# Kernel optimization log

Hardware: AMD Instinct MI355X
Metric: run time of the kernel (lower is better)

The kernel has to match this reference:

```python
import jax, jax.numpy as jnp
import numpy as np

B = 8192      # n_trials
N = 4096      # network size
N_IN = 3      # input channels (1 osc + 2 stim)
TAU = 0.1
DT = 0.0005


def setup_inputs() -> dict:
    key = jax.random.key(0)
    ks = jax.random.split(key, 8)
    k_t = jax.random.normal(ks[0], (B, 2), dtype=jnp.float32)
    phase = jax.random.uniform(ks[1], (B,), dtype=jnp.float32) * 2.0 * np.pi
    monodromy = jnp.tile(jnp.eye(2, dtype=jnp.float32)[None], (B, 1, 1))
    dK_norms = jnp.zeros((B,), dtype=jnp.float32)
    amp = jnp.float32(1.5)
    w = jnp.float32(2.0 * np.pi * 4.0)  # reference oscillation frequency
    stim = jax.random.normal(ks[2], (N_IN - 1,), dtype=jnp.float32)
    alpha = jax.random.normal(ks[3], (2, N_IN), dtype=jnp.float32)
    I = jax.random.normal(ks[4], (N_IN, N), dtype=jnp.float32)
    m = jax.random.normal(ks[5], (2, N), dtype=jnp.float32)
    n = jax.random.normal(ks[6], (2, N), dtype=jnp.float32)
    return {"k_t": k_t, "phase": phase, "monodromy": monodromy,
            "dK_norms": dK_norms, "amp": amp, "w": w, "stim": stim,
            "alpha": alpha, "I": I, "m": m, "n": n}


def reference(k_t, phase, monodromy, dK_norms, amp, w, stim, alpha, I, m, n):
    # calc_x_u
    tau_sw = w * TAU
    v_osc = amp / jnp.sqrt(1.0 + tau_sw ** 2) * jnp.sin(phase - jnp.arctan2(tau_sw, 1.0))  # [B]
    u_osc = amp * jnp.sin(phase)                                                           # [B]
    u_stim = jnp.broadcast_to(stim[None, :], (phase.shape[0], stim.shape[0]))              # [B, n_in-1]
    u = jnp.concatenate([u_osc[:, None], u_stim], axis=-1)                                  # [B, n_in]
    v = jnp.concatenate([v_osc[:, None], u_stim], axis=-1)                                  # [B, n_in]
    x = k_t @ m + v @ I                                                                     # [B, N]
    tx = jnp.tanh(x)
    # dKdt
    dK = (1.0 / TAU) * (-k_t + tx @ n.T / N + u @ alpha.T)                                  # [B, 2]
    # Jacobian: (1/tau) * (-I2 + (1/N) * einsum over neurons)
    dphi = 1.0 - tx ** 2                                                                    # [B, N]
    Jac = (1.0 / TAU) * (-jnp.eye(2, dtype=x.dtype)[None]
                         + jnp.einsum('bn,kn,dn->bkd', dphi, m, n) / N)                     # [B, 2, 2]
    # Euler update
    k_out = k_t + DT * dK
    phase_out = phase + DT * w
    mono_out = monodromy + DT * jnp.einsum('bkd,bde->bke', Jac, monodromy)
    dK_norms_out = dK_norms + jnp.linalg.norm(dK, axis=-1)
    return (k_out, phase_out, mono_out, dK_norms_out)
```

## Files before the change

### kernel.cpp

```cpp
#include <hip/hip_runtime.h>
#include <math.h>

#define N_SIZE 4096
#define B_SIZE 8192
#define T 4
#define NHALF 2048

typedef float v2f __attribute__((ext_vector_type(2)));

__device__ __forceinline__ float wave_sum(float v) {
#pragma unroll
    for (int off = 32; off >= 1; off >>= 1)
        v += __shfl_xor(v, off, 64);
    return v;
}

__device__ __forceinline__ v2f tanh2(v2f x) {
    v2f xe = x * 2.885390081777927f;
    v2f ex;
    ex.x = __builtin_amdgcn_exp2f(xe.x);
    ex.y = __builtin_amdgcn_exp2f(xe.y);
    v2f d = ex + 1.0f;
    v2f r;
    r.x = __builtin_amdgcn_rcpf(d.x);
    r.y = __builtin_amdgcn_rcpf(d.y);
    return 1.0f - 2.0f * r;
}

__global__ __launch_bounds__(1024)
void bif_kernel(const float* __restrict__ k_t,
                const float* __restrict__ phase,
                const float* __restrict__ mono,
                const float* __restrict__ dKn,
                const float* __restrict__ amp_p,
                const float* __restrict__ w_p,
                const float* __restrict__ stim,
                const float* __restrict__ alpha,
                const float* __restrict__ Im,
                const float* __restrict__ mm,
                const float* __restrict__ nm,
                float* __restrict__ out) {
    __shared__ float s_m0[N_SIZE], s_m1[N_SIZE], s_n0[N_SIZE], s_n1[N_SIZE];
    __shared__ float s_I0[N_SIZE], s_cv[N_SIZE];
    __shared__ float s_red[8 * 2 * 6 * T];

    const int tid  = threadIdx.x;
    const int lane = tid & 63;
    const int wvi  = tid >> 6;
    const int g    = wvi >> 1;
    const int h    = wvi & 1;
    const int b0   = blockIdx.x * 32 + g * T;

    const float st0 = stim[0];
    const float st1 = stim[1];

    {
        const int t4 = tid * 4;
        *(float4*)&s_m0[t4] = *(const float4*)&mm[t4];
        *(float4*)&s_m1[t4] = *(const float4*)&mm[N_SIZE + t4];
        *(float4*)&s_n0[t4] = *(const float4*)&nm[t4];
        *(float4*)&s_n1[t4] = *(const float4*)&nm[N_SIZE + t4];
        *(float4*)&s_I0[t4] = *(const float4*)&Im[t4];
        float4 i1 = *(const float4*)&Im[N_SIZE + t4];
        float4 i2 = *(const float4*)&Im[2 * N_SIZE + t4];
        float4 cv;
        cv.x = st0 * i1.x + st1 * i2.x;
        cv.y = st0 * i1.y + st1 * i2.y;
        cv.z = st0 * i1.z + st1 * i2.z;
        cv.w = st0 * i1.w + st1 * i2.w;
        *(float4*)&s_cv[t4] = cv;
    }

    const float amp = amp_p[0];
    const float w   = w_p[0];
    const float tau_sw = w * 0.1f;
    const float phi0 = atanf(tau_sw);
    const float vamp = amp / sqrtf(1.0f + tau_sw * tau_sw);

    float k0[T], k1[T], vo[T];
#pragma unroll
    for (int t = 0; t < T; ++t) {
        const int b = b0 + t;
        k0[t] = k_t[2 * b];
        k1[t] = k_t[2 * b + 1];
        vo[t] = vamp * sinf(phase[b] - phi0);
    }

    __syncthreads();

    v2f As0[T] = {}, As1[T] = {};
    v2f A00[T] = {}, A01[T] = {};
    v2f A10[T] = {}, A11[T] = {};

    const int base = h * NHALF;
#pragma unroll 2
    for (int it = 0; it < NHALF / 256; ++it) {
        const int j = base + it * 256 + lane * 4;
        float4 fm0 = *(const float4*)&s_m0[j];
        float4 fm1 = *(const float4*)&s_m1[j];
        float4 fn0 = *(const float4*)&s_n0[j];
        float4 fn1 = *(const float4*)&s_n1[j];
        float4 fi0 = *(const float4*)&s_I0[j];
        float4 fcv = *(const float4*)&s_cv[j];
        v2f Ms0[2] = {{fm0.x, fm0.y}, {fm0.z, fm0.w}};
        v2f Ms1[2] = {{fm1.x, fm1.y}, {fm1.z, fm1.w}};
        v2f Nn0[2] = {{fn0.x, fn0.y}, {fn0.z, fn0.w}};
        v2f Nn1[2] = {{fn1.x, fn1.y}, {fn1.z, fn1.w}};
        v2f Iv[2]  = {{fi0.x, fi0.y}, {fi0.z, fi0.w}};
        v2f Cv[2]  = {{fcv.x, fcv.y}, {fcv.z, fcv.w}};
#pragma unroll
        for (int p = 0; p < 2; ++p) {
#pragma unroll
            for (int t = 0; t < T; ++t) {
                v2f x  = Cv[p] + k0[t] * Ms0[p] + k1[t] * Ms1[p] + vo[t] * Iv[p];
                v2f tx = tanh2(x);
                v2f dphi = 1.0f - tx * tx;
                v2f a0 = dphi * Ms0[p];
                v2f a1 = dphi * Ms1[p];
                As0[t] += tx * Nn0[p];
                As1[t] += tx * Nn1[p];
                A00[t] += a0 * Nn0[p];
                A01[t] += a0 * Nn1[p];
                A10[t] += a1 * Nn0[p];
                A11[t] += a1 * Nn1[p];
            }
        }
    }

#pragma unroll
    for (int t = 0; t < T; ++t) {
        float r0 = wave_sum(As0[t].x + As0[t].y);
        float r1 = wave_sum(As1[t].x + As1[t].y);
        float r2 = wave_sum(A00[t].x + A00[t].y);
        float r3 = wave_sum(A01[t].x + A01[t].y);
        float r4 = wave_sum(A10[t].x + A10[t].y);
        float r5 = wave_sum(A11[t].x + A11[t].y);
        if (lane == 0) {
            float* rp = &s_red[((g * 2 + h) * 6) * T + t];
            rp[0 * T] = r0; rp[1 * T] = r1; rp[2 * T] = r2;
            rp[3 * T] = r3; rp[4 * T] = r4; rp[5 * T] = r5;
        }
    }
    __syncthreads();

    if (h == 0 && lane < T) {
        const int t = lane;
        const int b = b0 + t;
        const float* r0p = &s_red[((g * 2 + 0) * 6) * T + t];
        const float* r1p = &s_red[((g * 2 + 1) * 6) * T + t];
        float s0  = r0p[0 * T] + r1p[0 * T];
        float s1  = r0p[1 * T] + r1p[1 * T];
        float j00 = r0p[2 * T] + r1p[2 * T];
        float j01 = r0p[3 * T] + r1p[3 * T];
        float j10 = r0p[4 * T] + r1p[4 * T];
        float j11 = r0p[5 * T] + r1p[5 * T];

        const float kk0 = k_t[2 * b];
        const float kk1 = k_t[2 * b + 1];
        const float p   = phase[b];
        const float uo  = amp * sinf(p);
        const float a00 = alpha[0], a01 = alpha[1], a02 = alpha[2];
        const float a10 = alpha[3], a11 = alpha[4], a12 = alpha[5];
        const float invN = 1.0f / 4096.0f;
        const float DT = 0.0005f;

        float ua0 = uo * a00 + st0 * a01 + st1 * a02;
        float ua1 = uo * a10 + st0 * a11 + st1 * a12;
        float dK0 = 10.0f * (-kk0 + s0 * invN + ua0);
        float dK1 = 10.0f * (-kk1 + s1 * invN + ua1);
        out[2 * b]     = fmaf(DT, dK0, kk0);
        out[2 * b + 1] = fmaf(DT, dK1, kk1);
        out[B_SIZE * 2 + b] = p + DT * w;
        float J00 = 10.0f * (j00 * invN - 1.0f);
        float J01 = 10.0f * (j01 * invN);
        float J10 = 10.0f * (j10 * invN);
        float J11 = 10.0f * (j11 * invN - 1.0f);
        float M00 = mono[4 * b], M01 = mono[4 * b + 1];
        float M10 = mono[4 * b + 2], M11 = mono[4 * b + 3];
        float* om = out + B_SIZE * 3 + 4 * b;
        om[0] = M00 + DT * (J00 * M00 + J01 * M10);
        om[1] = M01 + DT * (J00 * M01 + J01 * M11);
        om[2] = M10 + DT * (J10 * M00 + J11 * M10);
        om[3] = M11 + DT * (J10 * M01 + J11 * M11);
        out[B_SIZE * 7 + b] = dKn[b] + sqrtf(dK0 * dK0 + dK1 * dK1);
    }
}

extern "C" void kernel_launch(void* const* d_in, const int* in_sizes, int n_in,
                              void* d_out, int out_size, void* d_ws, size_t ws_size,
                              hipStream_t stream) {
    const float* k_t   = (const float*)d_in[0];
    const float* phase = (const float*)d_in[1];
    const float* mono  = (const float*)d_in[2];
    const float* dKn   = (const float*)d_in[3];
    const float* amp   = (const float*)d_in[4];
    const float* w     = (const float*)d_in[5];
    const float* stim  = (const float*)d_in[6];
    const float* alpha = (const float*)d_in[7];
    const float* Im    = (const float*)d_in[8];
    const float* mm    = (const float*)d_in[9];
    const float* nm    = (const float*)d_in[10];
    float* out = (float*)d_out;

    bif_kernel<<<B_SIZE / 32, 1024, 0, stream>>>(
        k_t, phase, mono, dKn, amp, w, stim, alpha, Im, mm, nm, out);
}
```

Measured before the change: 24.73 us.

## Give each wave a full neuron range and fold exp2 scale into inputs

Each wave now processes all 4096 neurons for its 4 trials, which removes the half-split, the shared-memory partial reduction and the second barrier. Blocks shrink to 512 threads with a two-blocks-per-CU launch bound. The tanh exp2 scale constant is pre-multiplied into the stimulus term and per-trial coefficients to save a multiply per element, and epilogue global loads are hoisted before the main loop. The risk is that the 96KB LDS per block may prevent two blocks per CU, halving resident waves.

Result: no change. 25.09 us (+1.4%).

```diff
diff --git a/kernel.cpp b/kernel.cpp
--- a/kernel.cpp
+++ b/kernel.cpp
@@ -4,7 +4,7 @@
 #define N_SIZE 4096
 #define B_SIZE 8192
 #define T 4
-#define NHALF 2048
+#define C2L2E 2.885390081777927f
 
 typedef float v2f __attribute__((ext_vector_type(2)));
 
@@ -15,8 +15,7 @@
     return v;
 }
 
-__device__ __forceinline__ v2f tanh2(v2f x) {
-    v2f xe = x * 2.885390081777927f;
+__device__ __forceinline__ v2f tanh2_xe(v2f xe) {
     v2f ex;
     ex.x = __builtin_amdgcn_exp2f(xe.x);
     ex.y = __builtin_amdgcn_exp2f(xe.y);
@@ -27,7 +26,7 @@
     return 1.0f - 2.0f * r;
 }
 
-__global__ __launch_bounds__(1024)
+__global__ __launch_bounds__(512, 2)
 void bif_kernel(const float* __restrict__ k_t,
                 const float* __restrict__ phase,
                 const float* __restrict__ mono,
@@ -41,21 +40,19 @@
                 const float* __restrict__ nm,
                 float* __restrict__ out) {
     __shared__ float s_m0[N_SIZE], s_m1[N_SIZE], s_n0[N_SIZE], s_n1[N_SIZE];
-    __shared__ float s_I0[N_SIZE], s_cv[N_SIZE];
-    __shared__ float s_red[8 * 2 * 6 * T];
+    __shared__ float s_I0[N_SIZE], s_cvc[N_SIZE];
 
     const int tid  = threadIdx.x;
     const int lane = tid & 63;
-    const int wvi  = tid >> 6;
-    const int g    = wvi >> 1;
-    const int h    = wvi & 1;
-    const int b0   = blockIdx.x * 32 + g * T;
+    const int wid  = tid >> 6;
+    const int b0   = blockIdx.x * 32 + wid * T;
 
     const float st0 = stim[0];
     const float st1 = stim[1];
 
-    {
-        const int t4 = tid * 4;
+#pragma unroll
+    for (int h = 0; h < 2; ++h) {
+        const int t4 = h * 2048 + tid * 4;
         *(float4*)&s_m0[t4] = *(const float4*)&mm[t4];
         *(float4*)&s_m1[t4] = *(const float4*)&mm[N_SIZE + t4];
         *(float4*)&s_n0[t4] = *(const float4*)&nm[t4];
@@ -64,11 +61,11 @@
         float4 i1 = *(const float4*)&Im[N_SIZE + t4];
         float4 i2 = *(const float4*)&Im[2 * N_SIZE + t4];
         float4 cv;
-        cv.x = st0 * i1.x + st1 * i2.x;
-        cv.y = st0 * i1.y + st1 * i2.y;
-        cv.z = st0 * i1.z + st1 * i2.z;
-        cv.w = st0 * i1.w + st1 * i2.w;
-        *(float4*)&s_cv[t4] = cv;
+        cv.x = C2L2E * (st0 * i1.x + st1 * i2.x);
+        cv.y = C2L2E * (st0 * i1.y + st1 * i2.y);
+        cv.z = C2L2E * (st0 * i1.z + st1 * i2.z);
+        cv.w = C2L2E * (st0 * i1.w + st1 * i2.w);
+        *(float4*)&s_cvc[t4] = cv;
     }
 
     const float amp = amp_p[0];
@@ -77,13 +74,25 @@
     const float phi0 = atanf(tau_sw);
     const float vamp = amp / sqrtf(1.0f + tau_sw * tau_sw);
 
-    float k0[T], k1[T], vo[T];
+    float k0r[T], k1r[T];
+    float k0c[T], k1c[T], voc[T];
 #pragma unroll
     for (int t = 0; t < T; ++t) {
         const int b = b0 + t;
-        k0[t] = k_t[2 * b];
-        k1[t] = k_t[2 * b + 1];
-        vo[t] = vamp * sinf(phase[b] - phi0);
+        k0r[t] = k_t[2 * b];
+        k1r[t] = k_t[2 * b + 1];
+        k0c[t] = C2L2E * k0r[t];
+        k1c[t] = C2L2E * k1r[t];
+        voc[t] = C2L2E * vamp * sinf(phase[b] - phi0);
+    }
+
+    float  e_p = 0.f, e_dn = 0.f;
+    float4 e_mono = {0.f, 0.f, 0.f, 0.f};
+    if (lane < T) {
+        const int b = b0 + lane;
+        e_p  = phase[b];
+        e_dn = dKn[b];
+        e_mono = *(const float4*)&mono[4 * b];
     }
 
     __syncthreads();
@@ -92,16 +101,15 @@
     v2f A00[T] = {}, A01[T] = {};
     v2f A10[T] = {}, A11[T] = {};
 
-    const int base = h * NHALF;
-#pragma unroll 2
-    for (int it = 0; it < NHALF / 256; ++it) {
-        const int j = base + it * 256 + lane * 4;
+#pragma unroll 4
+    for (int it = 0; it < N_SIZE / 256; ++it) {
+        const int j = it * 256 + lane * 4;
         float4 fm0 = *(const float4*)&s_m0[j];
         float4 fm1 = *(const float4*)&s_m1[j];
         float4 fn0 = *(const float4*)&s_n0[j];
         float4 fn1 = *(const float4*)&s_n1[j];
         float4 fi0 = *(const float4*)&s_I0[j];
-        float4 fcv = *(const float4*)&s_cv[j];
+        float4 fcv = *(const float4*)&s_cvc[j];
         v2f Ms0[2] = {{fm0.x, fm0.y}, {fm0.z, fm0.w}};
         v2f Ms1[2] = {{fm1.x, fm1.y}, {fm1.z, fm1.w}};
         v2f Nn0[2] = {{fn0.x, fn0.y}, {fn0.z, fn0.w}};
@@ -112,8 +120,8 @@
         for (int p = 0; p < 2; ++p) {
 #pragma unroll
             for (int t = 0; t < T; ++t) {
-                v2f x  = Cv[p] + k0[t] * Ms0[p] + k1[t] * Ms1[p] + vo[t] * Iv[p];
-                v2f tx = tanh2(x);
+                v2f xe = Cv[p] + k0c[t] * Ms0[p] + k1c[t] * Ms1[p] + voc[t] * Iv[p];
+                v2f tx = tanh2_xe(xe);
                 v2f dphi = 1.0f - tx * tx;
                 v2f a0 = dphi * Ms0[p];
                 v2f a1 = dphi * Ms1[p];
@@ -127,38 +135,32 @@
         }
     }
 
+    float rs0[T], rs1[T], r00[T], r01[T], r10[T], r11[T];
 #pragma unroll
     for (int t = 0; t < T; ++t) {
-        float r0 = wave_sum(As0[t].x + As0[t].y);
-        float r1 = wave_sum(As1[t].x + As1[t].y);
-        float r2 = wave_sum(A00[t].x + A00[t].y);
-        float r3 = wave_sum(A01[t].x + A01[t].y);
-        float r4 = wave_sum(A10[t].x + A10[t].y);
-        float r5 = wave_sum(A11[t].x + A11[t].y);
-        if (lane == 0) {
-            float* rp = &s_red[((g * 2 + h) * 6) * T + t];
-            rp[0 * T] = r0; rp[1 * T] = r1; rp[2 * T] = r2;
-            rp[3 * T] = r3; rp[4 * T] = r4; rp[5 * T] = r5;
-        }
-    }
-    __syncthreads();
-
-    if (h == 0 && lane < T) {
+        rs0[t] = wave_sum(As0[t].x + As0[t].y);
+        rs1[t] = wave_sum(As1[t].x + As1[t].y);
+        r00[t] = wave_sum(A00[t].x + A00[t].y);
+        r01[t] = wave_sum(A01[t].x + A01[t].y);
+        r10[t] = wave_sum(A10[t].x + A10[t].y);
+        r11[t] = wave_sum(A11[t].x + A11[t].y);
+    }
+
+    if (lane < T) {
         const int t = lane;
         const int b = b0 + t;
-        const float* r0p = &s_red[((g * 2 + 0) * 6) * T + t];
-        const float* r1p = &s_red[((g * 2 + 1) * 6) * T + t];
-        float s0  = r0p[0 * T] + r1p[0 * T];
-        float s1  = r0p[1 * T] + r1p[1 * T];
-        float j00 = r0p[2 * T] + r1p[2 * T];
-        float j01 = r0p[3 * T] + r1p[3 * T];
-        float j10 = r0p[4 * T] + r1p[4 * T];
-        float j11 = r0p[5 * T] + r1p[5 * T];
-
-        const float kk0 = k_t[2 * b];
-        const float kk1 = k_t[2 * b + 1];
-        const float p   = phase[b];
-        const float uo  = amp * sinf(p);
+        float s0 = rs0[0], s1 = rs1[0], j00 = r00[0], j01 = r01[0], j10 = r10[0], j11 = r11[0];
+#pragma unroll
+        for (int q = 1; q < T; ++q) {
+            if (t == q) { s0 = rs0[q]; s1 = rs1[q]; j00 = r00[q]; j01 = r01[q]; j10 = r10[q]; j11 = r11[q]; }
+        }
+        float kk0 = k0r[0], kk1 = k1r[0];
+#pragma unroll
+        for (int q = 1; q < T; ++q) {
+            if (t == q) { kk0 = k0r[q]; kk1 = k1r[q]; }
+        }
+
+        const float uo  = amp * sinf(e_p);
         const float a00 = alpha[0], a01 = alpha[1], a02 = alpha[2];
         const float a10 = alpha[3], a11 = alpha[4], a12 = alpha[5];
         const float invN = 1.0f / 4096.0f;
@@ -170,19 +172,19 @@
         float dK1 = 10.0f * (-kk1 + s1 * invN + ua1);
         out[2 * b]     = fmaf(DT, dK0, kk0);
         out[2 * b + 1] = fmaf(DT, dK1, kk1);
-        out[B_SIZE * 2 + b] = p + DT * w;
+        out[B_SIZE * 2 + b] = e_p + DT * w;
         float J00 = 10.0f * (j00 * invN - 1.0f);
         float J01 = 10.0f * (j01 * invN);
         float J10 = 10.0f * (j10 * invN);
         float J11 = 10.0f * (j11 * invN - 1.0f);
-        float M00 = mono[4 * b], M01 = mono[4 * b + 1];
-        float M10 = mono[4 * b + 2], M11 = mono[4 * b + 3];
+        float M00 = e_mono.x, M01 = e_mono.y;
+        float M10 = e_mono.z, M11 = e_mono.w;
         float* om = out + B_SIZE * 3 + 4 * b;
         om[0] = M00 + DT * (J00 * M00 + J01 * M10);
         om[1] = M01 + DT * (J00 * M01 + J01 * M11);
         om[2] = M10 + DT * (J10 * M00 + J11 * M10);
         om[3] = M11 + DT * (J10 * M01 + J11 * M11);
-        out[B_SIZE * 7 + b] = dKn[b] + sqrtf(dK0 * dK0 + dK1 * dK1);
+        out[B_SIZE * 7 + b] = e_dn + sqrtf(dK0 * dK0 + dK1 * dK1);
     }
 }
 
@@ -202,6 +204,6 @@
     const float* nm    = (const float*)d_in[10];
     float* out = (float*)d_out;
 
-    bif_kernel<<<B_SIZE / 32, 1024, 0, stream>>>(
+    bif_kernel<<<B_SIZE / 32, 512, 0, stream>>>(
         k_t, phase, mono, dKn, amp, w, stim, alpha, Im, mm, nm, out);
 }
```
